# Performance work log

Measured on AMD Instinct MI355X. Metric: run time of the kernel, lower is better.

## Reference

```python
import jax, jax.numpy as jnp
import numpy as np

K = 4  # hard-coded in ParticleNet.__init__

# (fan_in, fan_out) for all linear layers
_DIMS = [(10, 32), (32, 64),        # edgeconv1 MLP (2*5 -> 32 -> 64)
         (128, 96), (96, 128),      # edgeconv2 MLP (2*64 -> 96 -> 128)
         (256, 192), (192, 256),    # edgeconv3 MLP (2*128 -> 192 -> 256)
         (453, 453), (453, 226), (226, 2)]  # output head (5+64+128+256=453)
_PNAMES = ['c1w1', 'c1w2', 'c2w1', 'c2w2', 'c3w1', 'c3w2', 'ow1', 'ow2', 'ow3']


def setup_inputs() -> dict:
    key = jax.random.key(0)
    ks = jax.random.split(key, 2 + len(_DIMS))
    inp = {
        'coords': jax.random.normal(ks[0], (1024, 128, 2), dtype=jnp.float32),
        'features': jax.random.normal(ks[1], (1024, 128, 5), dtype=jnp.float32),
    }
    for i, (name, (fi, fo)) in enumerate(zip(_PNAMES, _DIMS)):
        inp[name] = jax.random.normal(ks[2 + i], (fi, fo), dtype=jnp.float32) / np.sqrt(fi)
        inp[name.replace('w', 'b')] = jnp.zeros((fo,), dtype=jnp.float32)
    return inp


def _knn_idx(x, k):
    # x: [B,N,C] -> idx of k nearest neighbors (excluding self): [B,N,k]
    x2 = jnp.sum(x * x, axis=-1)                              # [B,N]
    d = x2[:, :, None] + x2[:, None, :] - 2.0 * jnp.einsum('bnc,bmc->bnm', x, x)
    d = d + jnp.eye(x.shape[1], dtype=x.dtype) * 1e9          # no self-loops
    _, idx = jax.lax.top_k(-d, k)
    return idx


def _edgeconv(x, idx, w1, b1, w2, b2):
    # EdgeConv: message = MLP([x_i, x_j - x_i]), mean-aggregated over k neighbors
    xj = jax.vmap(lambda xb, ib: xb[ib])(x, idx)              # [B,N,k,C]
    xi = jnp.broadcast_to(x[:, :, None, :], xj.shape)
    h = jnp.concatenate([xi, xj - xi], axis=-1)               # [B,N,k,2C]
    h = jax.nn.elu(h @ w1 + b1)
    h = jax.nn.elu(h @ w2 + b2)
    return jnp.mean(h, axis=2)                                # [B,N,out]


def reference(coords, features, c1w1, c1b1, c1w2, c1b2, c2w1, c2b1, c2w2, c2b2,
              c3w1, c3b1, c3w2, c3b2, ow1, ob1, ow2, ob2, ow3, ob3):
    idx1 = _knn_idx(coords, K)
    out1 = _edgeconv(features, idx1, c1w1, c1b1, c1w2, c1b2)  # [B,N,64]
    idx2 = _knn_idx(out1, K)
    out2 = _edgeconv(out1, idx2, c2w1, c2b1, c2w2, c2b2)      # [B,N,128]
    idx3 = _knn_idx(out2, K)
    out3 = _edgeconv(out2, idx3, c3w1, c3b1, c3w2, c3b2)      # [B,N,256]
    h = jnp.concatenate([features, out1, out2, out3], axis=-1)  # [B,N,453]
    h = jax.nn.elu(h @ ow1 + ob1)
    h = jax.nn.elu(h @ ow2 + ob2)
    return h @ ow3 + ob3                                      # [B,N,2]
```

## Files before the change

### kernel.cpp

```cpp
#include <hip/hip_runtime.h>
#include <cstdint>
#include <cstddef>


#define NB 1024
#define NPT 128

typedef __attribute__((ext_vector_type(8))) short short8;
typedef __attribute__((ext_vector_type(4))) float floatx4;
typedef __attribute__((ext_vector_type(4))) unsigned int uint4v;

__device__ __forceinline__ float elu_f(float x) { return x > 0.0f ? x : expm1f(x); }

__device__ __forceinline__ unsigned short f2bf(float f) {
  unsigned u = __builtin_bit_cast(unsigned, f);
  unsigned r = u + 0x7FFFu + ((u >> 16) & 1u);
  return (unsigned short)(r >> 16);
}
__device__ __forceinline__ float bf2f(unsigned short h) {
  unsigned u = ((unsigned)h) << 16;
  return __builtin_bit_cast(float, u);
}
__device__ __forceinline__ void split3(float v, unsigned short& h,
                                       unsigned short& m, unsigned short& l) {
  h = f2bf(v);
  float r = v - bf2f(h);
  m = f2bf(r);
  float r2 = r - bf2f(m);
  l = f2bf(r2);
}

#define INS6(dv, jv)                                                    \
  if ((dv) < bd5) {                                                     \
    bd5 = (dv); bi5 = (jv);                                             \
    if (bd5 < bd4) {                                                    \
      float _t = bd4; bd4 = bd5; bd5 = _t; int _i = bi4; bi4 = bi5; bi5 = _i; \
      if (bd4 < bd3) {                                                  \
        _t = bd3; bd3 = bd4; bd4 = _t; _i = bi3; bi3 = bi4; bi4 = _i;   \
        if (bd3 < bd2) {                                                \
          _t = bd2; bd2 = bd3; bd3 = _t; _i = bi2; bi2 = bi3; bi3 = _i; \
          if (bd2 < bd1) {                                              \
            _t = bd1; bd1 = bd2; bd2 = _t; _i = bi1; bi1 = bi2; bi2 = _i; \
            if (bd1 < bd0) {                                            \
              _t = bd0; bd0 = bd1; bd1 = _t; _i = bi0; bi0 = bi1; bi1 = _i; \
            } } } } } }

template<int C>
__global__ __launch_bounds__(128) void knn_kernel(const float* __restrict__ x,
                                                  int* __restrict__ idx) {
  __shared__ __align__(16) float xs[NPT][C + 4];
  __shared__ float x2s[NPT];
  __shared__ double x2d[NPT];
  const int b = blockIdx.x, t = threadIdx.x;
  const float* xb = x + (size_t)b * NPT * C;
  for (int e = t; e < NPT * C; e += 128) xs[e / C][e % C] = xb[e];
  __syncthreads();
  float xi[C];
  float s2 = 0.0f;
  double s2d = 0.0;
#pragma unroll
  for (int c = 0; c < C; ++c) {
    xi[c] = xs[t][c];
    s2 += xi[c] * xi[c];
    s2d += (double)xi[c] * (double)xi[c];
  }
  x2s[t] = s2;
  x2d[t] = s2d;
  __syncthreads();
  float bd0 = 1e30f, bd1 = 1e30f, bd2 = 1e30f, bd3 = 1e30f, bd4 = 1e30f, bd5 = 1e30f;
  int bi0 = 0, bi1 = 0, bi2 = 0, bi3 = 0, bi4 = 0, bi5 = 0;
  for (int j = 0; j < NPT; ++j) {
    if (j == t) continue;
    float dot = 0.0f;
#pragma unroll
    for (int c = 0; c < C; ++c) dot += xi[c] * xs[j][c];
    float d = s2 + x2s[j] - 2.0f * dot;
    INS6(d, j)
  }
  auto refine = [&](int j) -> double {
    double dot = 0.0;
#pragma unroll
    for (int c = 0; c < C; ++c) dot += (double)xi[c] * (double)xs[j][c];
    return s2d + x2d[j] - 2.0 * dot;
  };
  double e0 = refine(bi0), e1 = refine(bi1), e2 = refine(bi2);
  double e3 = refine(bi3), e4 = refine(bi4), e5 = refine(bi5);
#define CSWP(da, ia, db, ib)                                            \
  if ((da > db) || (da == db && ia > ib)) {                             \
    double _td = da; da = db; db = _td; int _ti = ia; ia = ib; ib = _ti; }
  CSWP(e0, bi0, e1, bi1) CSWP(e1, bi1, e2, bi2) CSWP(e2, bi2, e3, bi3)
  CSWP(e3, bi3, e4, bi4) CSWP(e4, bi4, e5, bi5)
  CSWP(e0, bi0, e1, bi1) CSWP(e1, bi1, e2, bi2) CSWP(e2, bi2, e3, bi3)
  CSWP(e3, bi3, e4, bi4)
  CSWP(e0, bi0, e1, bi1) CSWP(e1, bi1, e2, bi2) CSWP(e2, bi2, e3, bi3)
  CSWP(e0, bi0, e1, bi1) CSWP(e1, bi1, e2, bi2)
  CSWP(e0, bi0, e1, bi1)
#undef CSWP
  int* ib = idx + ((size_t)b * NPT + t) * 4;
  ib[0] = bi0; ib[1] = bi1; ib[2] = bi2; ib[3] = bi3;
}

template<int C>
__global__ __launch_bounds__(512) void knn_mfma_kernel(const float* __restrict__ x,
                                                       int* __restrict__ idx) {
  constexpr int KC = C / 32;
  constexpr int HS = C + 8;
  constexpr int FS = C + 4;
  constexpr int CQ = C / 4;
  __shared__ __align__(16) unsigned short lbuf[2 * NPT * HS];
  __shared__ float x2s[NPT];
  __shared__ double x2d[NPT];
  unsigned short* Xhi = lbuf;
  unsigned short* Xlo = lbuf + NPT * HS;
  float* Xs = reinterpret_cast<float*>(lbuf);
  const int b = blockIdx.x, t = threadIdx.x;
  const float* xb = x + (size_t)b * NPT * C;
  for (int e = t; e < NPT * C; e += 512) {
    int r = e / C, c = e % C;
    float v = xb[e];
    unsigned short h = f2bf(v);
    Xhi[r * HS + c] = h;
    Xlo[r * HS + c] = f2bf(v - bf2f(h));
  }
  {
    const int p = t >> 2, q = t & 3;
    const float4* r4 = reinterpret_cast<const float4*>(xb + p * C + q * CQ);
    float s2 = 0.f;
    double s2d = 0.0;
#pragma unroll
    for (int c4 = 0; c4 < CQ / 4; ++c4) {
      float4 v = r4[c4];
      s2 += v.x * v.x + v.y * v.y + v.z * v.z + v.w * v.w;
      s2d += (double)v.x * v.x + (double)v.y * v.y +
             (double)v.z * v.z + (double)v.w * v.w;
    }
    s2 += __shfl_xor(s2, 1);  s2 += __shfl_xor(s2, 2);
    s2d += __shfl_xor(s2d, 1); s2d += __shfl_xor(s2d, 2);
    if (q == 0) { x2s[p] = s2; x2d[p] = s2d; }
  }
  __syncthreads();
  const int w = t >> 6, l = t & 63;
  const int lr = l & 15, lq = l >> 4;
  const int iq = w * 16 + lr;
  short8 Bhi[KC], Blo[KC];
#pragma unroll
  for (int kk = 0; kk < KC; ++kk) {
    Bhi[kk] = *reinterpret_cast<const short8*>(&Xhi[iq * HS + kk * 32 + lq * 8]);
    Blo[kk] = *reinterpret_cast<const short8*>(&Xlo[iq * HS + kk * 32 + lq * 8]);
  }
  const float x2i = x2s[iq];
  float bd0 = 1e30f, bd1 = 1e30f, bd2 = 1e30f, bd3 = 1e30f, bd4 = 1e30f, bd5 = 1e30f;
  int bi0 = 0, bi1 = 0, bi2 = 0, bi3 = 0, bi4 = 0, bi5 = 0;
#pragma unroll
  for (int jt = 0; jt < 8; ++jt) {
    short8 Ahi[KC], Alo[KC];
#pragma unroll
    for (int kk = 0; kk < KC; ++kk) {
      Ahi[kk] = *reinterpret_cast<const short8*>(
          &Xhi[(jt * 16 + lr) * HS + kk * 32 + lq * 8]);
      Alo[kk] = *reinterpret_cast<const short8*>(
          &Xlo[(jt * 16 + lr) * HS + kk * 32 + lq * 8]);
    }
    floatx4 g = {0.f, 0.f, 0.f, 0.f};
#pragma unroll
    for (int kk = 0; kk < KC; ++kk) {
      g = __builtin_amdgcn_mfma_f32_16x16x32_bf16(Ahi[kk], Bhi[kk], g, 0, 0, 0);
      g = __builtin_amdgcn_mfma_f32_16x16x32_bf16(Ahi[kk], Blo[kk], g, 0, 0, 0);
      g = __builtin_amdgcn_mfma_f32_16x16x32_bf16(Alo[kk], Bhi[kk], g, 0, 0, 0);
    }
#pragma unroll
    for (int r = 0; r < 4; ++r) {
      int j = jt * 16 + lq * 4 + r;
      float d = (j == iq) ? 1e30f : (x2i + x2s[j] - 2.0f * g[r]);
      INS6(d, j)
    }
  }
#pragma unroll
  for (int rnd = 0; rnd < 2; ++rnd) {
    const int m = 16 << rnd;
    float od0 = __shfl_xor(bd0, m), od1 = __shfl_xor(bd1, m), od2 = __shfl_xor(bd2, m);
    float od3 = __shfl_xor(bd3, m), od4 = __shfl_xor(bd4, m), od5 = __shfl_xor(bd5, m);
    int oi0 = __shfl_xor(bi0, m), oi1 = __shfl_xor(bi1, m), oi2 = __shfl_xor(bi2, m);
    int oi3 = __shfl_xor(bi3, m), oi4 = __shfl_xor(bi4, m), oi5 = __shfl_xor(bi5, m);
    INS6(od0, oi0) INS6(od1, oi1) INS6(od2, oi2)
    INS6(od3, oi3) INS6(od4, oi4) INS6(od5, oi5)
  }
  bi0 = __shfl(bi0, lr); bi1 = __shfl(bi1, lr); bi2 = __shfl(bi2, lr);
  bi3 = __shfl(bi3, lr); bi4 = __shfl(bi4, lr); bi5 = __shfl(bi5, lr);
  __syncthreads();
  for (int e = t; e < NPT * C; e += 512) {
    int r = e / C, c = e % C;
    Xs[r * FS + c] = xb[e];
  }
  __syncthreads();
  const double x2di = x2d[iq];
  auto refine = [&](int j) -> double {
    double dot = 0.0;
    const float* ri = &Xs[iq * FS + lq * CQ];
    const float* rj = &Xs[j * FS + lq * CQ];
#pragma unroll
    for (int c = 0; c < CQ; ++c) dot += (double)ri[c] * (double)rj[c];
    dot += __shfl_xor(dot, 16);
    dot += __shfl_xor(dot, 32);
    return x2di + x2d[j] - 2.0 * dot;
  };
  double e0 = refine(bi0), e1 = refine(bi1), e2 = refine(bi2);
  double e3 = refine(bi3), e4 = refine(bi4), e5 = refine(bi5);
#define CSWP(da, ia, db, ib)                                            \
  if ((da > db) || (da == db && ia > ib)) {                             \
    double _td = da; da = db; db = _td; int _ti = ia; ia = ib; ib = _ti; }
  CSWP(e0, bi0, e1, bi1) CSWP(e1, bi1, e2, bi2) CSWP(e2, bi2, e3, bi3)
  CSWP(e3, bi3, e4, bi4) CSWP(e4, bi4, e5, bi5)
  CSWP(e0, bi0, e1, bi1) CSWP(e1, bi1, e2, bi2) CSWP(e2, bi2, e3, bi3)
  CSWP(e3, bi3, e4, bi4)
  CSWP(e0, bi0, e1, bi1) CSWP(e1, bi1, e2, bi2) CSWP(e2, bi2, e3, bi3)
  CSWP(e0, bi0, e1, bi1) CSWP(e1, bi1, e2, bi2)
  CSWP(e0, bi0, e1, bi1)
#undef CSWP
  if (lq == 0) {
    int* ib = idx + ((size_t)b * NPT + iq) * 4;
    ib[0] = bi0; ib[1] = bi1; ib[2] = bi2; ib[3] = bi3;
  }
}

__global__ __launch_bounds__(256) void ec1_kernel(
    const float* __restrict__ feat, const int* __restrict__ idx,
    const float* __restrict__ w1, const float* __restrict__ b1,
    const float* __restrict__ w2, const float* __restrict__ b2,
    float* __restrict__ out) {
  __shared__ __align__(16) float fs[NPT][6];
  __shared__ __align__(16) float w1s[10][32];
  __shared__ __align__(16) float w2s[32][68];
  __shared__ float hs[256][33];
  __shared__ float b1s[32], b2s[64];
  const int z = blockIdx.x, t = threadIdx.x;
  const int b = z >> 1, hh = z & 1;
  const float* fb = feat + (size_t)b * NPT * 5;
  for (int e = t; e < NPT * 5; e += 256) fs[e / 5][e % 5] = fb[e];
  for (int e = t; e < 320; e += 256) w1s[e / 32][e % 32] = w1[e];
  for (int e = t; e < 2048; e += 256) w2s[e >> 6][e & 63] = w2[e];
  if (t < 32) b1s[t] = b1[t];
  if (t >= 192) b2s[t - 192] = b2[t - 192];
  __syncthreads();
  {
    const int p = hh * 64 + (t >> 2);
    const int j = idx[(size_t)b * 512 + p * 4 + (t & 3)];
    float h[32];
#pragma unroll
    for (int o = 0; o < 32; ++o) h[o] = b1s[o];
#pragma unroll
    for (int c = 0; c < 10; ++c) {
      float in_c = (c < 5) ? fs[p][c] : (fs[j][c - 5] - fs[p][c - 5]);
      const float4* wr = reinterpret_cast<const float4*>(&w1s[c][0]);
#pragma unroll
      for (int o4 = 0; o4 < 8; ++o4) {
        float4 w = wr[o4];
        h[4 * o4 + 0] += in_c * w.x; h[4 * o4 + 1] += in_c * w.y;
        h[4 * o4 + 2] += in_c * w.z; h[4 * o4 + 3] += in_c * w.w;
      }
    }
#pragma unroll
    for (int o = 0; o < 32; ++o) hs[t][o] = elu_f(h[o]);
  }
  __syncthreads();
  {
    const int g = t >> 2, q = t & 3;
    const int o0 = q * 16;
    float acc[4][16];
#pragma unroll
    for (int m = 0; m < 16; ++m) {
      float bv = b2s[o0 + m];
#pragma unroll
      for (int i = 0; i < 4; ++i) acc[i][m] = bv;
    }
    for (int k = 0; k < 32; ++k) {
      float hk0 = hs[g * 4 + 0][k];
      float hk1 = hs[g * 4 + 1][k];
      float hk2 = hs[g * 4 + 2][k];
      float hk3 = hs[g * 4 + 3][k];
      const float4* wr = reinterpret_cast<const float4*>(&w2s[k][o0]);
#pragma unroll
      for (int m4 = 0; m4 < 4; ++m4) {
        float4 w = wr[m4];
        acc[0][4 * m4 + 0] += hk0 * w.x; acc[0][4 * m4 + 1] += hk0 * w.y;
        acc[0][4 * m4 + 2] += hk0 * w.z; acc[0][4 * m4 + 3] += hk0 * w.w;
        acc[1][4 * m4 + 0] += hk1 * w.x; acc[1][4 * m4 + 1] += hk1 * w.y;
        acc[1][4 * m4 + 2] += hk1 * w.z; acc[1][4 * m4 + 3] += hk1 * w.w;
        acc[2][4 * m4 + 0] += hk2 * w.x; acc[2][4 * m4 + 1] += hk2 * w.y;
        acc[2][4 * m4 + 2] += hk2 * w.z; acc[2][4 * m4 + 3] += hk2 * w.w;
        acc[3][4 * m4 + 0] += hk3 * w.x; acc[3][4 * m4 + 1] += hk3 * w.y;
        acc[3][4 * m4 + 2] += hk3 * w.z; acc[3][4 * m4 + 3] += hk3 * w.w;
      }
    }
    float* ob = out + ((size_t)b * NPT + hh * 64 + g) * 64 + o0;
#pragma unroll
    for (int m4 = 0; m4 < 4; ++m4) {
      float4 v;
      float* vp = &v.x;
#pragma unroll
      for (int s = 0; s < 4; ++s) {
        int m = 4 * m4 + s;
        vp[s] = 0.25f * (elu_f(acc[0][m]) + elu_f(acc[1][m]) +
                         elu_f(acc[2][m]) + elu_f(acc[3][m]));
      }
      *reinterpret_cast<float4*>(&ob[4 * m4]) = v;
    }
  }
}

__global__ __launch_bounds__(512, 2) void ec2a_kernel(
    const float* __restrict__ x, const int* __restrict__ idx,
    const float* __restrict__ w1, const float* __restrict__ b1,
    float* __restrict__ H) {
  __shared__ __align__(16) float xs[NPT][68];
  __shared__ __align__(16) float w1s[128][100];
  __shared__ float b1s[96];
  const int b = blockIdx.x, t = threadIdx.x;
  const float* xb = x + (size_t)b * NPT * 64;
  for (int e = t; e < NPT * 64; e += 512) xs[e >> 6][e & 63] = xb[e];
  for (int e = t; e < 128 * 96; e += 512) w1s[e / 96][e % 96] = w1[e];
  if (t < 96) b1s[t] = b1[t];
  __syncthreads();
  const int pb = t >> 2, part = t & 3;
  const int n0 = part * 24;
  int jn[4];
#pragma unroll
  for (int i = 0; i < 4; ++i) jn[i] = idx[(size_t)b * 512 + pb * 4 + i];
  float acc[4][24];
#pragma unroll
  for (int m = 0; m < 24; ++m) {
    float bv = b1s[n0 + m];
#pragma unroll
    for (int i = 0; i < 4; ++i) acc[i][m] = bv;
  }
  for (int c = 0; c < 64; ++c) {
    float in_c = xs[pb][c];
    const float4* wr = reinterpret_cast<const float4*>(&w1s[c][n0]);
#pragma unroll
    for (int q4 = 0; q4 < 6; ++q4) {
      float4 wv = wr[q4];
#pragma unroll
      for (int i = 0; i < 4; ++i) {
        acc[i][4 * q4 + 0] += in_c * wv.x;
        acc[i][4 * q4 + 1] += in_c * wv.y;
        acc[i][4 * q4 + 2] += in_c * wv.z;
        acc[i][4 * q4 + 3] += in_c * wv.w;
      }
    }
  }
  for (int c = 0; c < 64; ++c) {
    float xic = xs[pb][c];
    float in0 = xs[jn[0]][c] - xic;
    float in1 = xs[jn[1]][c] - xic;
    float in2 = xs[jn[2]][c] - xic;
    float in3 = xs[jn[3]][c] - xic;
    const float4* wr = reinterpret_cast<const float4*>(&w1s[64 + c][n0]);
#pragma unroll
    for (int q4 = 0; q4 < 6; ++q4) {
      float4 wv = wr[q4];
      acc[0][4 * q4 + 0] += in0 * wv.x; acc[0][4 * q4 + 1] += in0 * wv.y;
      acc[0][4 * q4 + 2] += in0 * wv.z; acc[0][4 * q4 + 3] += in0 * wv.w;
      acc[1][4 * q4 + 0] += in1 * wv.x; acc[1][4 * q4 + 1] += in1 * wv.y;
      acc[1][4 * q4 + 2] += in1 * wv.z; acc[1][4 * q4 + 3] += in1 * wv.w;
      acc[2][4 * q4 + 0] += in2 * wv.x; acc[2][4 * q4 + 1] += in2 * wv.y;
      acc[2][4 * q4 + 2] += in2 * wv.z; acc[2][4 * q4 + 3] += in2 * wv.w;
      acc[3][4 * q4 + 0] += in3 * wv.x; acc[3][4 * q4 + 1] += in3 * wv.y;
      acc[3][4 * q4 + 2] += in3 * wv.z; acc[3][4 * q4 + 3] += in3 * wv.w;
    }
  }
#pragma unroll
  for (int i = 0; i < 4; ++i) {
    float* hrow = H + ((size_t)b * 512 + pb * 4 + i) * 96 + n0;
#pragma unroll
    for (int q4 = 0; q4 < 6; ++q4) {
      float4 v = {elu_f(acc[i][4 * q4 + 0]), elu_f(acc[i][4 * q4 + 1]),
                  elu_f(acc[i][4 * q4 + 2]), elu_f(acc[i][4 * q4 + 3])};
      *reinterpret_cast<float4*>(&hrow[4 * q4]) = v;
    }
  }
}

__global__ __launch_bounds__(512) void ec2b_mfma_kernel(
    const float* __restrict__ H, const unsigned short* __restrict__ w2s3,
    const float* __restrict__ b2, float* __restrict__ out) {
  __shared__ __align__(16) unsigned short W[3 * 128 * 104];
  __shared__ float b2s[128];
  const int z = blockIdx.x, t = threadIdx.x;
  {
    const uint4v* src = reinterpret_cast<const uint4v*>(w2s3);
    uint4v* dst = reinterpret_cast<uint4v*>(W);
    for (int i = t; i < 3 * 128 * 104 / 8; i += 512) dst[i] = src[i];
  }
  if (t < 128) b2s[t] = b2[t];
  __syncthreads();
  const int w = t >> 6, l = t & 63;
  const int lr = l & 15, lq = l >> 4;
  for (int mt = 0; mt < 2; ++mt) {
    const int m = (w * 2 + mt) * 16;
    const size_t row = (size_t)z * 256 + m + lr;
    short8 Ah[3], Am[3], Al[3];
#pragma unroll
    for (int kk = 0; kk < 3; ++kk) {
      const float* s = &H[row * 96 + kk * 32 + lq * 8];
#pragma unroll
      for (int q = 0; q < 8; ++q) {
        unsigned short hh, mm, ll;
        split3(s[q], hh, mm, ll);
        Ah[kk][q] = (short)hh; Am[kk][q] = (short)mm; Al[kk][q] = (short)ll;
      }
    }
#pragma unroll
    for (int nt = 0; nt < 8; ++nt) {
      floatx4 acc = {0.f, 0.f, 0.f, 0.f};
#pragma unroll
      for (int kk = 0; kk < 3; ++kk) {
        const int off = (nt * 16 + lr) * 104 + kk * 32 + lq * 8;
        short8 Bh = *reinterpret_cast<const short8*>(&W[off]);
        short8 Bm = *reinterpret_cast<const short8*>(&W[128 * 104 + off]);
        short8 Bl = *reinterpret_cast<const short8*>(&W[2 * 128 * 104 + off]);
        acc = __builtin_amdgcn_mfma_f32_16x16x32_bf16(Ah[kk], Bh, acc, 0, 0, 0);
        acc = __builtin_amdgcn_mfma_f32_16x16x32_bf16(Ah[kk], Bm, acc, 0, 0, 0);
        acc = __builtin_amdgcn_mfma_f32_16x16x32_bf16(Am[kk], Bh, acc, 0, 0, 0);
        acc = __builtin_amdgcn_mfma_f32_16x16x32_bf16(Am[kk], Bm, acc, 0, 0, 0);
        acc = __builtin_amdgcn_mfma_f32_16x16x32_bf16(Ah[kk], Bl, acc, 0, 0, 0);
        acc = __builtin_amdgcn_mfma_f32_16x16x32_bf16(Al[kk], Bh, acc, 0, 0, 0);
      }
      const float bv = b2s[nt * 16 + lr];
      float s = elu_f(acc[0] + bv) + elu_f(acc[1] + bv) +
                elu_f(acc[2] + bv) + elu_f(acc[3] + bv);
      out[((size_t)z * 64 + (m >> 2) + lq) * 128 + nt * 16 + lr] = 0.25f * s;
    }
  }
}

__global__ __launch_bounds__(512, 2) void ec3a_kernel(
    const float* __restrict__ x, const int* __restrict__ idx,
    const unsigned short* __restrict__ w1t3g, const float* __restrict__ b1,
    unsigned short* __restrict__ h1) {
  __shared__ unsigned short Xb[128][136];
  __shared__ __align__(16) unsigned short W1t[192][264];
  __shared__ float b1s[192];
  __shared__ unsigned short stg[8][16][40];
  const int b = blockIdx.x, t = threadIdx.x;
  const float* xb = x + (size_t)b * NPT * 128;
  for (int e = t; e < NPT * 128; e += 512) Xb[e >> 7][e & 127] = f2bf(xb[e]);
  {
    const uint4v* src = reinterpret_cast<const uint4v*>(w1t3g);
    uint4v* dst = reinterpret_cast<uint4v*>(&W1t[0][0]);
    for (int i = t; i < 192 * 264 / 8; i += 512) dst[i] = src[i];
  }
  if (t < 192) b1s[t] = b1[t];
  __syncthreads();
  const int w = t >> 6, l = t & 63;
  const int lr = l & 15, lq = l >> 4;
  for (int mt = 0; mt < 4; ++mt) {
    const int m = (w * 4 + mt) * 16;
    const int e = m + lr;
    const int p = e >> 2;
    const int jp = idx[(size_t)b * 512 + e];
    short8 A[8];
#pragma unroll
    for (int kk = 0; kk < 4; ++kk) {
      int k0 = kk * 32 + lq * 8;
      A[kk] = *reinterpret_cast<const short8*>(&Xb[p][k0]);
    }
#pragma unroll
    for (int kk = 0; kk < 4; ++kk) {
      int k0 = kk * 32 + lq * 8;
      short8 aj = *reinterpret_cast<const short8*>(&Xb[jp][k0]);
      short8 ai = *reinterpret_cast<const short8*>(&Xb[p][k0]);
      short8 d;
#pragma unroll
      for (int q = 0; q < 8; ++q)
        d[q] = (short)f2bf(bf2f((unsigned short)aj[q]) - bf2f((unsigned short)ai[q]));
      A[4 + kk] = d;
    }
    floatx4 acc[12];
#pragma unroll
    for (int n = 0; n < 12; ++n) acc[n] = (floatx4){0.f, 0.f, 0.f, 0.f};
#pragma unroll
    for (int n = 0; n < 12; ++n) {
#pragma unroll
      for (int kk = 0; kk < 8; ++kk) {
        short8 Bf = *reinterpret_cast<const short8*>(&W1t[n * 16 + lr][kk * 32 + lq * 8]);
        acc[n] = __builtin_amdgcn_mfma_f32_16x16x32_bf16(A[kk], Bf, acc[n], 0, 0, 0);
      }
    }
#pragma unroll
    for (int pr = 0; pr < 6; ++pr) {
      float bv0 = b1s[pr * 32 + lr];
      float bv1 = b1s[pr * 32 + 16 + lr];
#pragma unroll
      for (int i = 0; i < 4; ++i) {
        stg[w][lq * 4 + i][lr]      = f2bf(elu_f(acc[2 * pr][i] + bv0));
        stg[w][lq * 4 + i][16 + lr] = f2bf(elu_f(acc[2 * pr + 1][i] + bv1));
      }
      asm volatile("s_waitcnt lgkmcnt(0)" ::: "memory");
      const unsigned short* src = &stg[w][l >> 2][(l & 3) * 8];
      uint4v vv = *reinterpret_cast<const uint4v*>(src);
      size_t dst = ((size_t)b * 512 + m + (l >> 2)) * 192 + pr * 32 + (l & 3) * 8;
      *reinterpret_cast<uint4v*>(&h1[dst]) = vv;
      asm volatile("s_waitcnt lgkmcnt(0)" ::: "memory");
    }
  }
}

__global__ __launch_bounds__(512, 2) void ec3b_kernel(
    const unsigned short* __restrict__ h1,
    const unsigned short* __restrict__ w2t3g, const float* __restrict__ b2,
    unsigned short* __restrict__ out3) {
  __shared__ __align__(16) unsigned short W2t[256][200];
  __shared__ float b2s[256];
  const int b = blockIdx.x, t = threadIdx.x;
  {
    const uint4v* src = reinterpret_cast<const uint4v*>(w2t3g);
    uint4v* dst = reinterpret_cast<uint4v*>(&W2t[0][0]);
    for (int i = t; i < 256 * 200 / 8; i += 512) dst[i] = src[i];
  }
  if (t < 256) b2s[t] = b2[t];
  __syncthreads();
  const int w = t >> 6, l = t & 63;
  const int lr = l & 15, lq = l >> 4;
  for (int mt = 0; mt < 4; ++mt) {
    const int m = (w * 4 + mt) * 16;
    floatx4 acc[16];
#pragma unroll
    for (int n = 0; n < 16; ++n) acc[n] = (floatx4){0.f, 0.f, 0.f, 0.f};
    const unsigned short* arow = h1 + ((size_t)b * 512 + m + lr) * 192;
#pragma unroll
    for (int kk = 0; kk < 6; ++kk) {
      short8 Af = *reinterpret_cast<const short8*>(&arow[kk * 32 + lq * 8]);
#pragma unroll
      for (int n = 0; n < 16; ++n) {
        short8 Bf = *reinterpret_cast<const short8*>(&W2t[n * 16 + lr][kk * 32 + lq * 8]);
        acc[n] = __builtin_amdgcn_mfma_f32_16x16x32_bf16(Af, Bf, acc[n], 0, 0, 0);
      }
    }
    unsigned short* orow = out3 + ((size_t)b * NPT + (m >> 2) + lq) * 256;
#pragma unroll
    for (int n = 0; n < 16; ++n) {
      float bv = b2s[n * 16 + lr];
      float s = 0.f;
#pragma unroll
      for (int i = 0; i < 4; ++i) s += elu_f(acc[n][i] + bv);
      orow[n * 16 + lr] = f2bf(0.25f * s);
    }
  }
}

__global__ __launch_bounds__(256) void prep_kernel(
    const float* __restrict__ hw1, const float* __restrict__ hw2,
    const float* __restrict__ c3w1, const float* __restrict__ c3w2,
    const float* __restrict__ c2w2,
    unsigned short* __restrict__ w1p, unsigned short* __restrict__ w2p,
    unsigned short* __restrict__ w1t3g, unsigned short* __restrict__ w2t3g,
    unsigned short* __restrict__ w2e2) {
  const int S0 = 512 * 480, S1 = S0 + 256 * 480, S2 = S1 + 192 * 264;
  const int S3 = S2 + 256 * 200, S4 = S3 + 3 * 128 * 104;
  int i = blockIdx.x * 256 + threadIdx.x;
  if (i < S0) {
    int n = i / 480, kp = i % 480;
    int ko = (kp < 5) ? kp : kp - 3;
    bool ok = ((kp < 5) || (kp >= 8 && kp < 456)) && (n < 453);
    w1p[i] = ok ? f2bf(hw1[(size_t)ko * 453 + n]) : (unsigned short)0;
  } else if (i < S1) {
    int j = i - S0;
    int n = j / 480, kp = j % 480;
    bool ok = (kp < 453) && (n < 226);
    w2p[j] = ok ? f2bf(hw2[(size_t)kp * 226 + n]) : (unsigned short)0;
  } else if (i < S2) {
    int m = i - S1;
    int n = m / 264, k = m % 264;
    w1t3g[m] = (k < 256) ? f2bf(c3w1[(size_t)k * 192 + n]) : (unsigned short)0;
  } else if (i < S3) {
    int m = i - S2;
    int n = m / 200, k = m % 200;
    w2t3g[m] = (k < 192) ? f2bf(c3w2[(size_t)k * 256 + n]) : (unsigned short)0;
  } else if (i < S4) {
    int m = i - S3;
    int s = m / (128 * 104), rem = m % (128 * 104);
    int n = rem / 104, k = rem % 104;
    float v = (k < 96) ? c2w2[(size_t)k * 128 + n] : 0.f;
    unsigned short hh, mm, ll;
    split3(v, hh, mm, ll);
    w2e2[m] = (s == 0) ? hh : (s == 1) ? mm : ll;
  }
}

#define HSTR 488
#define TPSS 72
__global__ __launch_bounds__(256, 2) void head_mfma_kernel(
    const float* __restrict__ feat, const float* __restrict__ o1,
    const float* __restrict__ o2, const unsigned short* __restrict__ o3,
    const unsigned short* __restrict__ w1p, const float* __restrict__ b1,
    const unsigned short* __restrict__ w2p, const float* __restrict__ b2,
    const float* __restrict__ w3, const float* __restrict__ b3,
    float* __restrict__ out) {
  __shared__ unsigned short uA[64 * HSTR];
  __shared__ __align__(16) unsigned short tps[4][16][TPSS];
  __shared__ float b1s[512], b2s[256], w3s[512];
  const int t = threadIdx.x;
  const size_t base = (size_t)blockIdx.x * 64;

  for (int i = t; i < 512; i += 256) b1s[i] = (i < 453) ? b1[i] : 0.f;
  if (t < 256) b2s[t] = (t < 226) ? b2[t] : 0.f;
  for (int i = t; i < 512; i += 256) w3s[i] = (i < 452) ? w3[i] : 0.f;

  const int w = t >> 6, l = t & 63;
  const int lr = l & 15, lq = l >> 4;
  const int tr = t >> 2, tc = t & 3;
  const size_t grow = base + w * 16 + lr;

  short8 Af[15];
#pragma unroll
  for (int kk = 0; kk < 15; ++kk) {
    const int kbase = kk * 32 + lq * 8;
    short8 r;
    if (kbase >= 456) {
#pragma unroll
      for (int q = 0; q < 8; ++q) r[q] = 0;
    } else if (kbase >= 200) {
      r = *reinterpret_cast<const short8*>(&o3[grow * 256 + (kbase - 200)]);
    } else if (kbase >= 72) {
      const float* s = &o2[grow * 128 + (kbase - 72)];
#pragma unroll
      for (int q = 0; q < 8; ++q) r[q] = (short)f2bf(s[q]);
    } else if (kbase >= 8) {
      const float* s = &o1[grow * 64 + (kbase - 8)];
#pragma unroll
      for (int q = 0; q < 8; ++q) r[q] = (short)f2bf(s[q]);
    } else {
      const float* s = &feat[grow * 5];
#pragma unroll
      for (int q = 0; q < 8; ++q) r[q] = (q < 5) ? (short)f2bf(s[q]) : (short)0;
    }
    Af[kk] = r;
  }

  uint4v v[15];
#define WLOAD(SRC, CH)                                                   \
  {                                                                      \
    _Pragma("unroll")                                                    \
    for (int i = 0; i < 15; ++i)                                         \
      v[i] = *reinterpret_cast<const uint4v*>(                           \
          &SRC[((size_t)((CH) * 64 + tr)) * 480 + (tc + 4 * i) * 8]);    \
  }
#define WWRITE()                                                         \
  {                                                                      \
    _Pragma("unroll")                                                    \
    for (int i = 0; i < 15; ++i)                                         \
      *reinterpret_cast<uint4v*>(&uA[tr * HSTR + (tc + 4 * i) * 8]) = v[i]; \
  }

  WLOAD(w1p, 0)
  WWRITE()
  __syncthreads();

  short8 Af2[15];
#pragma unroll
  for (int ch = 0; ch < 8; ++ch) {
    if (ch < 7) WLOAD(w1p, ch + 1)
    else       WLOAD(w2p, 0)
    floatx4 a0 = {0.f, 0.f, 0.f, 0.f}, a1 = {0.f, 0.f, 0.f, 0.f};
    floatx4 a2 = {0.f, 0.f, 0.f, 0.f}, a3 = {0.f, 0.f, 0.f, 0.f};
    __builtin_amdgcn_s_setprio(1);
#pragma unroll
    for (int kk = 0; kk < 15; ++kk) {
      int ko = kk * 32 + lq * 8;
      short8 B0 = *reinterpret_cast<const short8*>(&uA[(lr)*HSTR + ko]);
      short8 B1 = *reinterpret_cast<const short8*>(&uA[(16 + lr) * HSTR + ko]);
      short8 B2 = *reinterpret_cast<const short8*>(&uA[(32 + lr) * HSTR + ko]);
      short8 B3 = *reinterpret_cast<const short8*>(&uA[(48 + lr) * HSTR + ko]);
      a0 = __builtin_amdgcn_mfma_f32_16x16x32_bf16(Af[kk], B0, a0, 0, 0, 0);
      a1 = __builtin_amdgcn_mfma_f32_16x16x32_bf16(Af[kk], B1, a1, 0, 0, 0);
      a2 = __builtin_amdgcn_mfma_f32_16x16x32_bf16(Af[kk], B2, a2, 0, 0, 0);
      a3 = __builtin_amdgcn_mfma_f32_16x16x32_bf16(Af[kk], B3, a3, 0, 0, 0);
    }
    __builtin_amdgcn_s_setprio(0);
    {
      floatx4 aj[4] = {a0, a1, a2, a3};
#pragma unroll
      for (int jx = 0; jx < 4; ++jx) {
        int c = ch * 64 + jx * 16 + lr;
        float bb = b1s[c];
#pragma unroll
        for (int i = 0; i < 4; ++i)
          tps[w][lq * 4 + i][jx * 16 + lr] = f2bf(elu_f(aj[jx][i] + bb));
      }
    }
    asm volatile("s_waitcnt lgkmcnt(0)" ::: "memory");
    Af2[2 * ch] = *reinterpret_cast<const short8*>(&tps[w][lr][lq * 8]);
    if (ch < 7)
      Af2[2 * ch + 1] = *reinterpret_cast<const short8*>(&tps[w][lr][32 + lq * 8]);
    asm volatile("s_waitcnt lgkmcnt(0)" ::: "memory");
    __syncthreads();
    WWRITE()
    __syncthreads();
  }

  float p0[4] = {0.f, 0.f, 0.f, 0.f}, p1[4] = {0.f, 0.f, 0.f, 0.f};
#pragma unroll
  for (int ch = 0; ch < 4; ++ch) {
    if (ch < 3) WLOAD(w2p, ch + 1)
    floatx4 a0 = {0.f, 0.f, 0.f, 0.f}, a1 = {0.f, 0.f, 0.f, 0.f};
    floatx4 a2 = {0.f, 0.f, 0.f, 0.f}, a3 = {0.f, 0.f, 0.f, 0.f};
    __builtin_amdgcn_s_setprio(1);
#pragma unroll
    for (int kk = 0; kk < 15; ++kk) {
      int ko = kk * 32 + lq * 8;
      short8 B0 = *reinterpret_cast<const short8*>(&uA[(lr)*HSTR + ko]);
      short8 B1 = *reinterpret_cast<const short8*>(&uA[(16 + lr) * HSTR + ko]);
      short8 B2 = *reinterpret_cast<const short8*>(&uA[(32 + lr) * HSTR + ko]);
      short8 B3 = *reinterpret_cast<const short8*>(&uA[(48 + lr) * HSTR + ko]);
      a0 = __builtin_amdgcn_mfma_f32_16x16x32_bf16(Af2[kk], B0, a0, 0, 0, 0);
      a1 = __builtin_amdgcn_mfma_f32_16x16x32_bf16(Af2[kk], B1, a1, 0, 0, 0);
      a2 = __builtin_amdgcn_mfma_f32_16x16x32_bf16(Af2[kk], B2, a2, 0, 0, 0);
      a3 = __builtin_amdgcn_mfma_f32_16x16x32_bf16(Af2[kk], B3, a3, 0, 0, 0);
    }
    __builtin_amdgcn_s_setprio(0);
    {
      floatx4 aj[4] = {a0, a1, a2, a3};
#pragma unroll
      for (int jx = 0; jx < 4; ++jx) {
        int c = ch * 64 + jx * 16 + lr;
        float bb = b2s[c];
        float wa = w3s[2 * c], wb = w3s[2 * c + 1];
#pragma unroll
        for (int i = 0; i < 4; ++i) {
          float h = (c < 226) ? elu_f(aj[jx][i] + bb) : 0.f;
          p0[i] += h * wa;
          p1[i] += h * wb;
        }
      }
    }
    if (ch < 3) {
      __syncthreads();
      WWRITE()
      __syncthreads();
    }
  }

#pragma unroll
  for (int i = 0; i < 4; ++i) {
    float a = p0[i], bvv = p1[i];
#pragma unroll
    for (int m = 1; m < 16; m <<= 1) {
      a += __shfl_xor(a, m);
      bvv += __shfl_xor(bvv, m);
    }
    if (lr == 0) {
      size_t row = base + w * 16 + lq * 4 + i;
      float2 vv = {a + b3[0], bvv + b3[1]};
      *reinterpret_cast<float2*>(&out[row * 2]) = vv;
    }
  }
#undef WLOAD
#undef WWRITE
}

extern "C" void kernel_launch(void* const* d_in, const int* in_sizes, int n_in,
                              void* d_out, int out_size, void* d_ws, size_t ws_size,
                              hipStream_t stream) {
  const float* coords = (const float*)d_in[0];
  const float* feat   = (const float*)d_in[1];
  const float* c1w1 = (const float*)d_in[2];  const float* c1b1 = (const float*)d_in[3];
  const float* c1w2 = (const float*)d_in[4];  const float* c1b2 = (const float*)d_in[5];
  const float* c2w1 = (const float*)d_in[6];  const float* c2b1 = (const float*)d_in[7];
  const float* c2w2 = (const float*)d_in[8];  const float* c2b2 = (const float*)d_in[9];
  const float* c3w1 = (const float*)d_in[10]; const float* c3b1 = (const float*)d_in[11];
  const float* c3w2 = (const float*)d_in[12]; const float* c3b2 = (const float*)d_in[13];
  const float* ow1  = (const float*)d_in[14]; const float* ob1  = (const float*)d_in[15];
  const float* ow2  = (const float*)d_in[16]; const float* ob2  = (const float*)d_in[17];
  const float* ow3  = (const float*)d_in[18]; const float* ob3  = (const float*)d_in[19];
  float* out = (float*)d_out;

  char* ws = (char*)d_ws;
  float* out1 = (float*)(ws);
  float* out2 = (float*)(ws + (32ull << 20));
  unsigned short* out3b = (unsigned short*)(ws + (96ull << 20));
  float* Hbuf2 = (float*)(ws + (96ull << 20));
  unsigned short* h1 = (unsigned short*)(ws + (162ull << 20));
  unsigned short* w1p = (unsigned short*)(ws + (212ull << 20));
  unsigned short* w2p = (unsigned short*)(ws + (212ull << 20) + (512ull << 10));
  unsigned short* w1t3g = (unsigned short*)(ws + (213ull << 20));
  unsigned short* w2t3g = (unsigned short*)(ws + (213ull << 20) + (256ull << 10));
  int* idx = (int*)(ws + (214ull << 20));
  unsigned short* w2e2 = (unsigned short*)(ws + (216ull << 20));

  prep_kernel<<<1994, 256, 0, stream>>>(ow1, ow2, c3w1, c3w2, c2w2,
                                        w1p, w2p, w1t3g, w2t3g, w2e2);
  knn_kernel<2><<<NB, 128, 0, stream>>>(coords, idx);
  ec1_kernel<<<2 * NB, 256, 0, stream>>>(feat, idx, c1w1, c1b1, c1w2, c1b2, out1);
  knn_mfma_kernel<64><<<NB, 512, 0, stream>>>(out1, idx);
  for (int c = 0; c < 2; ++c) {
    ec2a_kernel<<<512, 512, 0, stream>>>(out1 + (size_t)c * 512 * NPT * 64,
                                         idx + (size_t)c * 512 * 512,
                                         c2w1, c2b1, Hbuf2);
    ec2b_mfma_kernel<<<1024, 512, 0, stream>>>(Hbuf2, w2e2, c2b2,
                                               out2 + (size_t)c * 512 * NPT * 128);
  }
  knn_mfma_kernel<128><<<NB, 512, 0, stream>>>(out2, idx);
  for (int c = 0; c < 4; ++c) {
    ec3a_kernel<<<256, 512, 0, stream>>>(out2 + (size_t)c * 256 * NPT * 128,
                                         idx + (size_t)c * 256 * 512,
                                         w1t3g, c3b1, h1);
    ec3b_kernel<<<256, 512, 0, stream>>>(h1, w2t3g, c3b2,
                                         out3b + (size_t)c * 256 * NPT * 256);
  }
  head_mfma_kernel<<<2048, 256, 0, stream>>>(feat, out1, out2, out3b,
                                             w1p, ob1, w2p, ob2, ow3, ob3, out);
}
```

Measured before the change: 1.717 ms.

## Move edgeconv2 first layer to bf16x3 split MFMA

Replaces the FP32 scalar FMA implementation of edgeconv2's first linear layer with MFMA bf16 matrix instructions. It keeps near-fp32 accuracy by splitting both activations and weights into three bf16 parts. The prep kernel now also builds the split, transposed weight buffer for c2w1. This aims to cut the ALU-bound cost of the 128->96 matmul per edge, at the price of six MFMAs per k-step, split conversion work in-kernel, and scalar (non-vectorized) stores to H.

```diff
diff --git a/kernel.cpp b/kernel.cpp
--- a/kernel.cpp
+++ b/kernel.cpp
@@ -308,74 +308,63 @@
   }
 }
 
-__global__ __launch_bounds__(512, 2) void ec2a_kernel(
+__global__ __launch_bounds__(512) void ec2a_mfma_kernel(
     const float* __restrict__ x, const int* __restrict__ idx,
-    const float* __restrict__ w1, const float* __restrict__ b1,
+    const unsigned short* __restrict__ w1s3, const float* __restrict__ b1,
     float* __restrict__ H) {
-  __shared__ __align__(16) float xs[NPT][68];
-  __shared__ __align__(16) float w1s[128][100];
+  __shared__ __align__(16) float Xs[NPT][68];
+  __shared__ __align__(16) unsigned short W[3 * 96 * 136];
   __shared__ float b1s[96];
   const int b = blockIdx.x, t = threadIdx.x;
   const float* xb = x + (size_t)b * NPT * 64;
-  for (int e = t; e < NPT * 64; e += 512) xs[e >> 6][e & 63] = xb[e];
-  for (int e = t; e < 128 * 96; e += 512) w1s[e / 96][e % 96] = w1[e];
+  for (int e = t; e < NPT * 64; e += 512) Xs[e >> 6][e & 63] = xb[e];
+  {
+    const uint4v* src = reinterpret_cast<const uint4v*>(w1s3);
+    uint4v* dst = reinterpret_cast<uint4v*>(W);
+    for (int i = t; i < 3 * 96 * 136 / 8; i += 512) dst[i] = src[i];
+  }
   if (t < 96) b1s[t] = b1[t];
   __syncthreads();
-  const int pb = t >> 2, part = t & 3;
-  const int n0 = part * 24;
-  int jn[4];
-#pragma unroll
-  for (int i = 0; i < 4; ++i) jn[i] = idx[(size_t)b * 512 + pb * 4 + i];
-  float acc[4][24];
-#pragma unroll
-  for (int m = 0; m < 24; ++m) {
-    float bv = b1s[n0 + m];
-#pragma unroll
-    for (int i = 0; i < 4; ++i) acc[i][m] = bv;
-  }
-  for (int c = 0; c < 64; ++c) {
-    float in_c = xs[pb][c];
-    const float4* wr = reinterpret_cast<const float4*>(&w1s[c][n0]);
-#pragma unroll
-    for (int q4 = 0; q4 < 6; ++q4) {
-      float4 wv = wr[q4];
-#pragma unroll
-      for (int i = 0; i < 4; ++i) {
-        acc[i][4 * q4 + 0] += in_c * wv.x;
-        acc[i][4 * q4 + 1] += in_c * wv.y;
-        acc[i][4 * q4 + 2] += in_c * wv.z;
-        acc[i][4 * q4 + 3] += in_c * wv.w;
-      }
-    }
-  }
-  for (int c = 0; c < 64; ++c) {
-    float xic = xs[pb][c];
-    float in0 = xs[jn[0]][c] - xic;
-    float in1 = xs[jn[1]][c] - xic;
-    float in2 = xs[jn[2]][c] - xic;
-    float in3 = xs[jn[3]][c] - xic;
-    const float4* wr = reinterpret_cast<const float4*>(&w1s[64 + c][n0]);
-#pragma unroll
-    for (int q4 = 0; q4 < 6; ++q4) {
-      float4 wv = wr[q4];
-      acc[0][4 * q4 + 0] += in0 * wv.x; acc[0][4 * q4 + 1] += in0 * wv.y;
-      acc[0][4 * q4 + 2] += in0 * wv.z; acc[0][4 * q4 + 3] += in0 * wv.w;
-      acc[1][4 * q4 + 0] += in1 * wv.x; acc[1][4 * q4 + 1] += in1 * wv.y;
-      acc[1][4 * q4 + 2] += in1 * wv.z; acc[1][4 * q4 + 3] += in1 * wv.w;
-      acc[2][4 * q4 + 0] += in2 * wv.x; acc[2][4 * q4 + 1] += in2 * wv.y;
-      acc[2][4 * q4 + 2] += in2 * wv.z; acc[2][4 * q4 + 3] += in2 * wv.w;
-      acc[3][4 * q4 + 0] += in3 * wv.x; acc[3][4 * q4 + 1] += in3 * wv.y;
-      acc[3][4 * q4 + 2] += in3 * wv.z; acc[3][4 * q4 + 3] += in3 * wv.w;
-    }
-  }
-#pragma unroll
-  for (int i = 0; i < 4; ++i) {
-    float* hrow = H + ((size_t)b * 512 + pb * 4 + i) * 96 + n0;
-#pragma unroll
-    for (int q4 = 0; q4 < 6; ++q4) {
-      float4 v = {elu_f(acc[i][4 * q4 + 0]), elu_f(acc[i][4 * q4 + 1]),
-                  elu_f(acc[i][4 * q4 + 2]), elu_f(acc[i][4 * q4 + 3])};
-      *reinterpret_cast<float4*>(&hrow[4 * q4]) = v;
+  const int w = t >> 6, l = t & 63;
+  const int lr = l & 15, lq = l >> 4;
+  for (int mt = 0; mt < 4; ++mt) {
+    const int m = (w * 4 + mt) * 16;
+    const int e = m + lr;
+    const int p = e >> 2;
+    const int j = idx[(size_t)b * 512 + e];
+    short8 Ah[4], Am[4], Al[4];
+#pragma unroll
+    for (int kk = 0; kk < 4; ++kk) {
+#pragma unroll
+      for (int q = 0; q < 8; ++q) {
+        int c = (kk & 1) * 32 + lq * 8 + q;
+        float v = (kk < 2) ? Xs[p][c] : (Xs[j][c] - Xs[p][c]);
+        unsigned short hh, mm, ll;
+        split3(v, hh, mm, ll);
+        Ah[kk][q] = (short)hh; Am[kk][q] = (short)mm; Al[kk][q] = (short)ll;
+      }
+    }
+#pragma unroll
+    for (int nt = 0; nt < 6; ++nt) {
+      floatx4 acc = {0.f, 0.f, 0.f, 0.f};
+#pragma unroll
+      for (int kk = 0; kk < 4; ++kk) {
+        const int off = (nt * 16 + lr) * 136 + kk * 32 + lq * 8;
+        short8 Bh = *reinterpret_cast<const short8*>(&W[off]);
+        short8 Bm = *reinterpret_cast<const short8*>(&W[96 * 136 + off]);
+        short8 Bl = *reinterpret_cast<const short8*>(&W[2 * 96 * 136 + off]);
+        acc = __builtin_amdgcn_mfma_f32_16x16x32_bf16(Ah[kk], Bh, acc, 0, 0, 0);
+        acc = __builtin_amdgcn_mfma_f32_16x16x32_bf16(Ah[kk], Bm, acc, 0, 0, 0);
+        acc = __builtin_amdgcn_mfma_f32_16x16x32_bf16(Am[kk], Bh, acc, 0, 0, 0);
+        acc = __builtin_amdgcn_mfma_f32_16x16x32_bf16(Am[kk], Bm, acc, 0, 0, 0);
+        acc = __builtin_amdgcn_mfma_f32_16x16x32_bf16(Ah[kk], Bl, acc, 0, 0, 0);
+        acc = __builtin_amdgcn_mfma_f32_16x16x32_bf16(Al[kk], Bh, acc, 0, 0, 0);
+      }
+      const float bv = b1s[nt * 16 + lr];
+#pragma unroll
+      for (int i = 0; i < 4; ++i)
+        H[((size_t)b * 512 + m + lq * 4 + i) * 96 + nt * 16 + lr] =
+            elu_f(acc[i] + bv);
     }
   }
 }
@@ -551,12 +540,12 @@
 __global__ __launch_bounds__(256) void prep_kernel(
     const float* __restrict__ hw1, const float* __restrict__ hw2,
     const float* __restrict__ c3w1, const float* __restrict__ c3w2,
-    const float* __restrict__ c2w2,
+    const float* __restrict__ c2w1, const float* __restrict__ c2w2,
     unsigned short* __restrict__ w1p, unsigned short* __restrict__ w2p,
     unsigned short* __restrict__ w1t3g, unsigned short* __restrict__ w2t3g,
-    unsigned short* __restrict__ w2e2) {
+    unsigned short* __restrict__ w1e2, unsigned short* __restrict__ w2e2) {
   const int S0 = 512 * 480, S1 = S0 + 256 * 480, S2 = S1 + 192 * 264;
-  const int S3 = S2 + 256 * 200, S4 = S3 + 3 * 128 * 104;
+  const int S3 = S2 + 256 * 200, S4 = S3 + 3 * 96 * 136, S5 = S4 + 3 * 128 * 104;
   int i = blockIdx.x * 256 + threadIdx.x;
   if (i < S0) {
     int n = i / 480, kp = i % 480;
@@ -578,6 +567,14 @@
     w2t3g[m] = (k < 192) ? f2bf(c3w2[(size_t)k * 256 + n]) : (unsigned short)0;
   } else if (i < S4) {
     int m = i - S3;
+    int s = m / (96 * 136), rem = m % (96 * 136);
+    int n = rem / 136, k = rem % 136;
+    float v = (k < 128) ? c2w1[(size_t)k * 96 + n] : 0.f;
+    unsigned short hh, mm, ll;
+    split3(v, hh, mm, ll);
+    w1e2[m] = (s == 0) ? hh : (s == 1) ? mm : ll;
+  } else if (i < S5) {
+    int m = i - S4;
     int s = m / (128 * 104), rem = m % (128 * 104);
     int n = rem / 104, k = rem % 104;
     float v = (k < 96) ? c2w2[(size_t)k * 128 + n] : 0.f;
@@ -785,17 +782,18 @@
   unsigned short* w1t3g = (unsigned short*)(ws + (213ull << 20));
   unsigned short* w2t3g = (unsigned short*)(ws + (213ull << 20) + (256ull << 10));
   int* idx = (int*)(ws + (214ull << 20));
-  unsigned short* w2e2 = (unsigned short*)(ws + (216ull << 20));
-
-  prep_kernel<<<1994, 256, 0, stream>>>(ow1, ow2, c3w1, c3w2, c2w2,
-                                        w1p, w2p, w1t3g, w2t3g, w2e2);
+  unsigned short* w1e2 = (unsigned short*)(ws + (216ull << 20));
+  unsigned short* w2e2 = (unsigned short*)(ws + (217ull << 20));
+
+  prep_kernel<<<2147, 256, 0, stream>>>(ow1, ow2, c3w1, c3w2, c2w1, c2w2,
+                                        w1p, w2p, w1t3g, w2t3g, w1e2, w2e2);
   knn_kernel<2><<<NB, 128, 0, stream>>>(coords, idx);
   ec1_kernel<<<2 * NB, 256, 0, stream>>>(feat, idx, c1w1, c1b1, c1w2, c1b2, out1);
   knn_mfma_kernel<64><<<NB, 512, 0, stream>>>(out1, idx);
   for (int c = 0; c < 2; ++c) {
-    ec2a_kernel<<<512, 512, 0, stream>>>(out1 + (size_t)c * 512 * NPT * 64,
-                                         idx + (size_t)c * 512 * 512,
-                                         c2w1, c2b1, Hbuf2);
+    ec2a_mfma_kernel<<<512, 512, 0, stream>>>(out1 + (size_t)c * 512 * NPT * 64,
+                                              idx + (size_t)c * 512 * 512,
+                                              w1e2, c2b1, Hbuf2);
     ec2b_mfma_kernel<<<1024, 512, 0, stream>>>(Hbuf2, w2e2, c2b2,
                                                out2 + (size_t)c * 512 * NPT * 128);
   }
```

Result: slower. 1.853 ms (+7.9%).
